# Optimization experiments

Measured on AMD Instinct MI355X. Metric: run time of the kernel, lower is better.

## Reference

```python
import jax, jax.numpy as jnp
import numpy as np

N = 8192
E = 262144
IN_DIM, HID_DIM, Z_DIM = 512, 256, 64


def setup_inputs() -> dict:
    key = jax.random.key(0)
    ks = jax.random.split(key, 8)
    x = jax.random.normal(ks[0], (N, IN_DIM), dtype=jnp.float32)
    edge_src = jax.random.randint(ks[1], (E,), 0, N, dtype=jnp.int32)
    edge_dst = jax.random.randint(ks[2], (E,), 0, N, dtype=jnp.int32)
    edge_w = jax.random.uniform(ks[3], (E,), dtype=jnp.float32)
    eps = jax.random.normal(ks[4], (N, Z_DIM), dtype=jnp.float32)
    # xavier-uniform linear weights (stored [in, out]); biases zero (as in torch init)
    def xavier(k, fan_in, fan_out):
        lim = float(np.sqrt(6.0 / (fan_in + fan_out)))
        return jax.random.uniform(k, (fan_in, fan_out), minval=-lim, maxval=lim, dtype=jnp.float32)
    W1 = xavier(ks[5], IN_DIM, HID_DIM)
    b1 = jnp.zeros((HID_DIM,), dtype=jnp.float32)
    Wmu = xavier(ks[6], HID_DIM, Z_DIM)
    bmu = jnp.zeros((Z_DIM,), dtype=jnp.float32)
    Wls = xavier(ks[7], HID_DIM, Z_DIM)
    bls = jnp.zeros((Z_DIM,), dtype=jnp.float32)
    return {"x": x, "edge_src": edge_src, "edge_dst": edge_dst, "edge_w": edge_w,
            "eps": eps, "W1": W1, "b1": b1, "Wmu": Wmu, "bmu": bmu, "Wls": Wls, "bls": bls}


def _spmm(edge_src, edge_dst, edge_w, h):
    # out[i] = sum_{(i,j) in edges} w_ij * h[j]  == torch.spmm(adj, h)
    return jax.ops.segment_sum(edge_w[:, None] * h[edge_dst], edge_src, num_segments=N)


def reference(x, edge_src, edge_dst, edge_w, eps, W1, b1, Wmu, bmu, Wls, bls):
    # GCN layer 1: linear -> spmm -> tanh
    h = jnp.tanh(_spmm(edge_src, edge_dst, edge_w, x @ W1 + b1))
    # mu / logstd heads (no activation)
    mu = _spmm(edge_src, edge_dst, edge_w, h @ Wmu + bmu)
    logstd = _spmm(edge_src, edge_dst, edge_w, h @ Wls + bls)
    # reparameterize (training mode): z = mu + eps * exp(logstd)
    z = mu + eps * jnp.exp(logstd)
    # inner-product decoder
    adj_logits = z @ z.T  # [N, N]
    return (z, adj_logits, mu, logstd)
```

## Files before the change

kernel.cpp:

```cpp
#include <hip/hip_runtime.h>
#include <math.h>

#define IN_DIM 512
#define HID    256
#define ZD     64

typedef short bf16x8 __attribute__((ext_vector_type(8)));
typedef float f32x4  __attribute__((ext_vector_type(4)));


__global__ void k_zero_int(int* p, int n) {
    int i = blockIdx.x * blockDim.x + threadIdx.x;
    if (i < n) p[i] = 0;
}

__global__ void k_count(const int* __restrict__ src, int* __restrict__ deg, int E) {
    int e = blockIdx.x * blockDim.x + threadIdx.x;
    if (e < E) atomicAdd(&deg[src[e]], 1);
}

__global__ __launch_bounds__(256) void k_scan(const int* __restrict__ deg,
                                              int* __restrict__ rp,
                                              int* __restrict__ nxt, int N) {
    __shared__ int sums[256];
    int t = threadIdx.x;
    int chunk = N / 256;
    int base = t * chunk;
    int run = 0;
    for (int i = 0; i < chunk; ++i) run += deg[base + i];
    sums[t] = run;
    __syncthreads();
    for (int off = 1; off < 256; off <<= 1) {
        int u = (t >= off) ? sums[t - off] : 0;
        __syncthreads();
        sums[t] += u;
        __syncthreads();
    }
    int excl = (t == 0) ? 0 : sums[t - 1];
    int run2 = excl;
    for (int i = 0; i < chunk; ++i) {
        rp[base + i]  = run2;
        nxt[base + i] = run2;
        run2 += deg[base + i];
    }
    if (t == 255) rp[N] = run2;
}

__global__ void k_scatter(const int* __restrict__ src, const int* __restrict__ dst,
                          const float* __restrict__ w, int* __restrict__ nxt,
                          int* __restrict__ col, float* __restrict__ wv, int E) {
    int e = blockIdx.x * blockDim.x + threadIdx.x;
    if (e < E) {
        int pos = atomicAdd(&nxt[src[e]], 1);
        col[pos] = dst[e];
        wv[pos]  = w[e];
    }
}

__global__ __launch_bounds__(256) void k_gemm1(const float* __restrict__ x,
                                               const float* __restrict__ W1,
                                               const float* __restrict__ b1,
                                               float* __restrict__ h0) {
    __shared__ float As[16][68];
    __shared__ float Bs[16][68];
    int tx = threadIdx.x, ty = threadIdx.y;
    int t = ty * 16 + tx;
    int rowBase = blockIdx.y * 64, colBase = blockIdx.x * 64;
    float acc[4][4] = {};
    int kk_l = t & 15, m0 = t >> 4;
    int c_l = t & 63, k_l = t >> 6;
    for (int k0 = 0; k0 < IN_DIM; k0 += 16) {
        #pragma unroll
        for (int p = 0; p < 4; ++p) {
            int m = m0 + p * 16;
            As[kk_l][m] = x[(size_t)(rowBase + m) * IN_DIM + k0 + kk_l];
        }
        #pragma unroll
        for (int p = 0; p < 4; ++p) {
            int kk = k_l + p * 4;
            Bs[kk][c_l] = W1[(size_t)(k0 + kk) * HID + colBase + c_l];
        }
        __syncthreads();
        #pragma unroll
        for (int kk = 0; kk < 16; ++kk) {
            float4 a4 = *(const float4*)&As[kk][ty * 4];
            float4 b4 = *(const float4*)&Bs[kk][tx * 4];
            float a[4] = {a4.x, a4.y, a4.z, a4.w};
            float b[4] = {b4.x, b4.y, b4.z, b4.w};
            #pragma unroll
            for (int r = 0; r < 4; ++r)
                #pragma unroll
                for (int c = 0; c < 4; ++c)
                    acc[r][c] += a[r] * b[c];
        }
        __syncthreads();
    }
    float4 bias = *(const float4*)&b1[colBase + tx * 4];
    float bb[4] = {bias.x, bias.y, bias.z, bias.w};
    #pragma unroll
    for (int r = 0; r < 4; ++r) {
        float4 o;
        o.x = acc[r][0] + bb[0];
        o.y = acc[r][1] + bb[1];
        o.z = acc[r][2] + bb[2];
        o.w = acc[r][3] + bb[3];
        *(float4*)&h0[(size_t)(rowBase + ty * 4 + r) * HID + colBase + tx * 4] = o;
    }
}

__global__ __launch_bounds__(256) void k_spmm_tanh(const int* __restrict__ rp,
                                                   const int* __restrict__ col,
                                                   const float* __restrict__ wv,
                                                   const float* __restrict__ h0,
                                                   float* __restrict__ h) {
    __shared__ int scol[256];
    __shared__ float sw[256];
    int i = blockIdx.x, t = threadIdx.x;
    int s = rp[i], e = rp[i + 1];
    float acc = 0.f;
    for (int cs = s; cs < e; cs += 256) {
        int n = min(256, e - cs);
        __syncthreads();
        if (t < n) { scol[t] = col[cs + t]; sw[t] = wv[cs + t]; }
        __syncthreads();
        #pragma unroll 4
        for (int p = 0; p < n; ++p)
            acc += sw[p] * h0[(size_t)scol[p] * HID + t];
    }
    h[(size_t)i * HID + t] = tanhf(acc);
}

__global__ __launch_bounds__(256) void k_heads(const float* __restrict__ h,
                                               const float* __restrict__ Wmu,
                                               const float* __restrict__ bmu,
                                               const float* __restrict__ Wls,
                                               const float* __restrict__ bls,
                                               float* __restrict__ hm,
                                               float* __restrict__ hl) {
    __shared__ float ht[16][HID + 1];
    int t = threadIdx.x;
    int rowBase = blockIdx.x * 16;
    #pragma unroll
    for (int p = 0; p < 16; ++p)
        ht[p][t] = h[(size_t)(rowBase + p) * HID + t];
    __syncthreads();
    int c = t & 63, rg = t >> 6;
    float amu[4] = {}, als[4] = {};
    #pragma unroll 4
    for (int k = 0; k < HID; ++k) {
        float wm = Wmu[k * ZD + c];
        float wl = Wls[k * ZD + c];
        #pragma unroll
        for (int r = 0; r < 4; ++r) {
            float hv = ht[rg * 4 + r][k];
            amu[r] += hv * wm;
            als[r] += hv * wl;
        }
    }
    float bm = bmu[c], bl = bls[c];
    #pragma unroll
    for (int r = 0; r < 4; ++r) {
        int row = rowBase + rg * 4 + r;
        hm[(size_t)row * ZD + c] = amu[r] + bm;
        hl[(size_t)row * ZD + c] = als[r] + bl;
    }
}

__global__ __launch_bounds__(64) void k_spmm_heads(const int* __restrict__ rp,
                                                   const int* __restrict__ col,
                                                   const float* __restrict__ wv,
                                                   const float* __restrict__ hm,
                                                   const float* __restrict__ hl,
                                                   const float* __restrict__ eps,
                                                   float* __restrict__ mu,
                                                   float* __restrict__ ls,
                                                   float* __restrict__ z) {
    __shared__ int scol[64];
    __shared__ float sw[64];
    int i = blockIdx.x, t = threadIdx.x;
    int s = rp[i], e = rp[i + 1];
    float amu = 0.f, als = 0.f;
    for (int cs = s; cs < e; cs += 64) {
        int n = min(64, e - cs);
        __syncthreads();
        if (t < n) { scol[t] = col[cs + t]; sw[t] = wv[cs + t]; }
        __syncthreads();
        #pragma unroll 4
        for (int p = 0; p < n; ++p) {
            size_t off = (size_t)scol[p] * ZD + t;
            float w = sw[p];
            amu += w * hm[off];
            als += w * hl[off];
        }
    }
    size_t o = (size_t)i * ZD + t;
    mu[o] = amu;
    ls[o] = als;
    z[o]  = amu + eps[o] * expf(als);
}

__global__ void k_cvt_bf16(const float* __restrict__ z, unsigned short* __restrict__ zb, int n4) {
    int i = blockIdx.x * blockDim.x + threadIdx.x;
    if (i < n4) {
        float4 v = *(const float4*)&z[i * 4];
        float vv[4] = {v.x, v.y, v.z, v.w};
        ushort4 o;
        unsigned short* op = (unsigned short*)&o;
        #pragma unroll
        for (int j = 0; j < 4; ++j) {
            unsigned int b = __float_as_uint(vv[j]);
            b += 0x7FFFu + ((b >> 16) & 1u);
            op[j] = (unsigned short)(b >> 16);
        }
        *(ushort4*)&zb[i * 4] = o;
    }
}

__global__ __launch_bounds__(256) void k_zzt_mfma(const unsigned short* __restrict__ zb,
                                                  float* __restrict__ out, int N) {
    int lane = threadIdx.x & 63;
    int w    = threadIdx.x >> 6;
    int waveRow = blockIdx.y * 128 + (w >> 1) * 64;
    int waveCol = blockIdx.x * 128 + (w & 1) * 64;
    int m    = lane & 15;
    int quad = lane >> 4;
    int kofs = quad * 8;

    bf16x8 a[4][2], b[4][2];
    #pragma unroll
    for (int rg = 0; rg < 4; ++rg) {
        const unsigned short* pr = zb + (size_t)(waveRow + rg * 16 + m) * ZD + kofs;
        const unsigned short* pc = zb + (size_t)(waveCol + rg * 16 + m) * ZD + kofs;
        a[rg][0] = *(const bf16x8*)pr;
        a[rg][1] = *(const bf16x8*)(pr + 32);
        b[rg][0] = *(const bf16x8*)pc;
        b[rg][1] = *(const bf16x8*)(pc + 32);
    }

    f32x4 acc[4][4] = {};
    #pragma unroll
    for (int rg = 0; rg < 4; ++rg)
        #pragma unroll
        for (int cg = 0; cg < 4; ++cg) {
            acc[rg][cg] = __builtin_amdgcn_mfma_f32_16x16x32_bf16(a[rg][0], b[cg][0], acc[rg][cg], 0, 0, 0);
            acc[rg][cg] = __builtin_amdgcn_mfma_f32_16x16x32_bf16(a[rg][1], b[cg][1], acc[rg][cg], 0, 0, 0);
        }

    #pragma unroll
    for (int rg = 0; rg < 4; ++rg) {
        int row0 = waveRow + rg * 16 + quad * 4;
        #pragma unroll
        for (int cg = 0; cg < 4; ++cg) {
            int c = waveCol + cg * 16 + m;
            #pragma unroll
            for (int r = 0; r < 4; ++r)
                out[(size_t)(row0 + r) * N + c] = acc[rg][cg][r];
        }
    }
}


extern "C" void kernel_launch(void* const* d_in, const int* in_sizes, int n_in,
                              void* d_out, int out_size, void* d_ws, size_t ws_size,
                              hipStream_t stream) {
    const float* x    = (const float*)d_in[0];
    const int*   esrc = (const int*)d_in[1];
    const int*   edst = (const int*)d_in[2];
    const float* ew   = (const float*)d_in[3];
    const float* eps  = (const float*)d_in[4];
    const float* W1   = (const float*)d_in[5];
    const float* b1   = (const float*)d_in[6];
    const float* Wmu  = (const float*)d_in[7];
    const float* bmu  = (const float*)d_in[8];
    const float* Wls  = (const float*)d_in[9];
    const float* bls  = (const float*)d_in[10];
    int N = in_sizes[0] / IN_DIM;
    int E = in_sizes[1];

    float* h0 = (float*)d_ws;
    float* h  = h0 + (size_t)N * HID;
    float* hm = h  + (size_t)N * HID;
    float* hl = hm + (size_t)N * ZD;
    int* rp   = (int*)(hl + (size_t)N * ZD);
    int* deg  = rp + (N + 1);
    int* nxt  = deg + N;
    int* col  = nxt + N;
    float* wv = (float*)(col + E);
    unsigned short* zb = (unsigned short*)(wv + E);

    float* out_z   = (float*)d_out;
    float* out_adj = out_z + (size_t)N * ZD;
    float* out_mu  = out_adj + (size_t)N * N;
    float* out_ls  = out_mu + (size_t)N * ZD;

    k_zero_int<<<(N + 255) / 256, 256, 0, stream>>>(deg, N);
    k_count<<<(E + 255) / 256, 256, 0, stream>>>(esrc, deg, E);
    k_scan<<<1, 256, 0, stream>>>(deg, rp, nxt, N);
    k_scatter<<<(E + 255) / 256, 256, 0, stream>>>(esrc, edst, ew, nxt, col, wv, E);

    dim3 b16(16, 16);
    dim3 g1(HID / 64, N / 64);
    k_gemm1<<<g1, b16, 0, stream>>>(x, W1, b1, h0);

    k_spmm_tanh<<<N, 256, 0, stream>>>(rp, col, wv, h0, h);

    k_heads<<<N / 16, 256, 0, stream>>>(h, Wmu, bmu, Wls, bls, hm, hl);

    k_spmm_heads<<<N, 64, 0, stream>>>(rp, col, wv, hm, hl, eps, out_mu, out_ls, out_z);

    k_cvt_bf16<<<(N * ZD / 4 + 255) / 256, 256, 0, stream>>>(out_z, zb, N * ZD / 4);

    dim3 g2(N / 128, N / 128);
    k_zzt_mfma<<<g2, 256, 0, stream>>>(zb, out_adj, N);
}
```

Measured before the change: 461.0 us.

## Move layer-1 GEMM to split-bf16 MFMA and fuse heads spmm with bf16 cast

Replaces the fp32 SIMT GEMM for x@W1 with a bf16x3 MFMA GEMM: x is split into hi/lo bf16 parts, W1 is transposed and split the same way, and three MFMAs per tile keep accuracy close to fp32. The mu and logstd heads are interleaved into one 128-wide buffer, so a single spmm gathers both and also writes the bf16 copy of z, which removes the separate conversion kernel. The z·zᵀ output is now written as non-temporal 16-byte vector stores using a swapped MFMA operand order. The extra split and transpose kernels add memory traffic and launch overhead in exchange.

```diff
diff --git a/kernel.cpp b/kernel.cpp
--- a/kernel.cpp
+++ b/kernel.cpp
@@ -7,6 +7,15 @@
 
 typedef short bf16x8 __attribute__((ext_vector_type(8)));
 typedef float f32x4  __attribute__((ext_vector_type(4)));
+
+__device__ inline unsigned short f2bf_rne(float f) {
+    unsigned int b = __float_as_uint(f);
+    b += 0x7FFFu + ((b >> 16) & 1u);
+    return (unsigned short)(b >> 16);
+}
+__device__ inline float bf2f(unsigned short h) {
+    return __uint_as_float(((unsigned int)h) << 16);
+}
 
 
 __global__ void k_zero_int(int* p, int n) {
@@ -57,54 +66,98 @@
     }
 }
 
-__global__ __launch_bounds__(256) void k_gemm1(const float* __restrict__ x,
-                                               const float* __restrict__ W1,
-                                               const float* __restrict__ b1,
-                                               float* __restrict__ h0) {
-    __shared__ float As[16][68];
-    __shared__ float Bs[16][68];
+__global__ void k_split_x(const float* __restrict__ x,
+                          unsigned short* __restrict__ xh,
+                          unsigned short* __restrict__ xl, int n4) {
+    int i = blockIdx.x * blockDim.x + threadIdx.x;
+    if (i < n4) {
+        float4 v = *(const float4*)&x[(size_t)i * 4];
+        float vv[4] = {v.x, v.y, v.z, v.w};
+        ushort4 ho, lo;
+        unsigned short* hp = (unsigned short*)&ho;
+        unsigned short* lp = (unsigned short*)&lo;
+        #pragma unroll
+        for (int j = 0; j < 4; ++j) {
+            unsigned short hcur = f2bf_rne(vv[j]);
+            hp[j] = hcur;
+            lp[j] = f2bf_rne(vv[j] - bf2f(hcur));
+        }
+        *(ushort4*)&xh[(size_t)i * 4] = ho;
+        *(ushort4*)&xl[(size_t)i * 4] = lo;
+    }
+}
+
+__global__ __launch_bounds__(256) void k_trans_w(const float* __restrict__ W,
+                                                 unsigned short* __restrict__ Wt_h,
+                                                 unsigned short* __restrict__ Wt_l,
+                                                 int K, int Nw) {
+    __shared__ float tile[32][33];
+    int n0 = blockIdx.x * 32, k0 = blockIdx.y * 32;
     int tx = threadIdx.x, ty = threadIdx.y;
-    int t = ty * 16 + tx;
-    int rowBase = blockIdx.y * 64, colBase = blockIdx.x * 64;
-    float acc[4][4] = {};
-    int kk_l = t & 15, m0 = t >> 4;
-    int c_l = t & 63, k_l = t >> 6;
-    for (int k0 = 0; k0 < IN_DIM; k0 += 16) {
-        #pragma unroll
-        for (int p = 0; p < 4; ++p) {
-            int m = m0 + p * 16;
-            As[kk_l][m] = x[(size_t)(rowBase + m) * IN_DIM + k0 + kk_l];
-        }
-        #pragma unroll
-        for (int p = 0; p < 4; ++p) {
-            int kk = k_l + p * 4;
-            Bs[kk][c_l] = W1[(size_t)(k0 + kk) * HID + colBase + c_l];
-        }
-        __syncthreads();
-        #pragma unroll
-        for (int kk = 0; kk < 16; ++kk) {
-            float4 a4 = *(const float4*)&As[kk][ty * 4];
-            float4 b4 = *(const float4*)&Bs[kk][tx * 4];
-            float a[4] = {a4.x, a4.y, a4.z, a4.w};
-            float b[4] = {b4.x, b4.y, b4.z, b4.w};
+    #pragma unroll
+    for (int j = 0; j < 4; ++j) {
+        int k = ty + j * 8;
+        tile[k][tx] = W[(size_t)(k0 + k) * Nw + n0 + tx];
+    }
+    __syncthreads();
+    #pragma unroll
+    for (int j = 0; j < 4; ++j) {
+        int n = ty + j * 8;
+        float v = tile[tx][n];
+        size_t o = (size_t)(n0 + n) * K + k0 + tx;
+        unsigned short hcur = f2bf_rne(v);
+        Wt_h[o] = hcur;
+        Wt_l[o] = f2bf_rne(v - bf2f(hcur));
+    }
+}
+
+__global__ __launch_bounds__(256) void k_gemm1_mfma(const unsigned short* __restrict__ xh,
+                                                    const unsigned short* __restrict__ xl,
+                                                    const unsigned short* __restrict__ wth,
+                                                    const unsigned short* __restrict__ wtl,
+                                                    const float* __restrict__ b1,
+                                                    float* __restrict__ h0) {
+    int lane = threadIdx.x & 63;
+    int w    = threadIdx.x >> 6;
+    int rowBase = blockIdx.y * 64 + (w >> 1) * 32;
+    int colBase = blockIdx.x * 64 + (w & 1) * 32;
+    int m    = lane & 15;
+    int quad = lane >> 4;
+    int kofs = quad * 8;
+
+    f32x4 acc[2][2] = {};
+    #pragma unroll 2
+    for (int k0 = 0; k0 < IN_DIM; k0 += 32) {
+        bf16x8 xhf[2], xlf[2], whf[2], wlf[2];
+        #pragma unroll
+        for (int g = 0; g < 2; ++g) {
+            size_t xoff = (size_t)(rowBase + g * 16 + m) * IN_DIM + k0 + kofs;
+            xhf[g] = *(const bf16x8*)&xh[xoff];
+            xlf[g] = *(const bf16x8*)&xl[xoff];
+            size_t woff = (size_t)(colBase + g * 16 + m) * IN_DIM + k0 + kofs;
+            whf[g] = *(const bf16x8*)&wth[woff];
+            wlf[g] = *(const bf16x8*)&wtl[woff];
+        }
+        #pragma unroll
+        for (int xg = 0; xg < 2; ++xg)
             #pragma unroll
-            for (int r = 0; r < 4; ++r)
-                #pragma unroll
-                for (int c = 0; c < 4; ++c)
-                    acc[r][c] += a[r] * b[c];
-        }
-        __syncthreads();
-    }
-    float4 bias = *(const float4*)&b1[colBase + tx * 4];
-    float bb[4] = {bias.x, bias.y, bias.z, bias.w};
-    #pragma unroll
-    for (int r = 0; r < 4; ++r) {
-        float4 o;
-        o.x = acc[r][0] + bb[0];
-        o.y = acc[r][1] + bb[1];
-        o.z = acc[r][2] + bb[2];
-        o.w = acc[r][3] + bb[3];
-        *(float4*)&h0[(size_t)(rowBase + ty * 4 + r) * HID + colBase + tx * 4] = o;
+            for (int wg = 0; wg < 2; ++wg) {
+                acc[xg][wg] = __builtin_amdgcn_mfma_f32_16x16x32_bf16(whf[wg], xhf[xg], acc[xg][wg], 0, 0, 0);
+                acc[xg][wg] = __builtin_amdgcn_mfma_f32_16x16x32_bf16(whf[wg], xlf[xg], acc[xg][wg], 0, 0, 0);
+                acc[xg][wg] = __builtin_amdgcn_mfma_f32_16x16x32_bf16(wlf[wg], xhf[xg], acc[xg][wg], 0, 0, 0);
+            }
+    }
+    #pragma unroll
+    for (int wg = 0; wg < 2; ++wg) {
+        float4 bv = *(const float4*)&b1[colBase + wg * 16 + quad * 4];
+        float bb[4] = {bv.x, bv.y, bv.z, bv.w};
+        #pragma unroll
+        for (int xg = 0; xg < 2; ++xg) {
+            f32x4 o = acc[xg][wg];
+            #pragma unroll
+            for (int r = 0; r < 4; ++r) o[r] += bb[r];
+            *(f32x4*)&h0[(size_t)(rowBase + xg * 16 + m) * HID + colBase + wg * 16 + quad * 4] = o;
+        }
     }
 }
 
@@ -135,9 +188,8 @@
                                                const float* __restrict__ bmu,
                                                const float* __restrict__ Wls,
                                                const float* __restrict__ bls,
-                                               float* __restrict__ hm,
-                                               float* __restrict__ hl) {
-    __shared__ float ht[16][HID + 1];
+                                               float* __restrict__ hh) {
+    __shared__ float ht[16][HID + 4];
     int t = threadIdx.x;
     int rowBase = blockIdx.x * 16;
     #pragma unroll
@@ -146,73 +198,65 @@
     __syncthreads();
     int c = t & 63, rg = t >> 6;
     float amu[4] = {}, als[4] = {};
-    #pragma unroll 4
-    for (int k = 0; k < HID; ++k) {
-        float wm = Wmu[k * ZD + c];
-        float wl = Wls[k * ZD + c];
+    for (int k = 0; k < HID; k += 4) {
+        float hv[4][4];
         #pragma unroll
         for (int r = 0; r < 4; ++r) {
-            float hv = ht[rg * 4 + r][k];
-            amu[r] += hv * wm;
-            als[r] += hv * wl;
+            float4 tmp = *(const float4*)&ht[rg * 4 + r][k];
+            hv[r][0] = tmp.x; hv[r][1] = tmp.y; hv[r][2] = tmp.z; hv[r][3] = tmp.w;
+        }
+        #pragma unroll
+        for (int j = 0; j < 4; ++j) {
+            float wm = Wmu[(k + j) * ZD + c];
+            float wl = Wls[(k + j) * ZD + c];
+            #pragma unroll
+            for (int r = 0; r < 4; ++r) {
+                amu[r] += hv[r][j] * wm;
+                als[r] += hv[r][j] * wl;
+            }
         }
     }
     float bm = bmu[c], bl = bls[c];
     #pragma unroll
     for (int r = 0; r < 4; ++r) {
         int row = rowBase + rg * 4 + r;
-        hm[(size_t)row * ZD + c] = amu[r] + bm;
-        hl[(size_t)row * ZD + c] = als[r] + bl;
-    }
-}
-
-__global__ __launch_bounds__(64) void k_spmm_heads(const int* __restrict__ rp,
-                                                   const int* __restrict__ col,
-                                                   const float* __restrict__ wv,
-                                                   const float* __restrict__ hm,
-                                                   const float* __restrict__ hl,
-                                                   const float* __restrict__ eps,
-                                                   float* __restrict__ mu,
-                                                   float* __restrict__ ls,
-                                                   float* __restrict__ z) {
-    __shared__ int scol[64];
-    __shared__ float sw[64];
+        hh[(size_t)row * 128 + c]      = amu[r] + bm;
+        hh[(size_t)row * 128 + 64 + c] = als[r] + bl;
+    }
+}
+
+__global__ __launch_bounds__(128) void k_spmm_heads(const int* __restrict__ rp,
+                                                    const int* __restrict__ col,
+                                                    const float* __restrict__ wv,
+                                                    const float* __restrict__ hh,
+                                                    const float* __restrict__ eps,
+                                                    float* __restrict__ mu,
+                                                    float* __restrict__ ls,
+                                                    float* __restrict__ z,
+                                                    unsigned short* __restrict__ zb) {
+    __shared__ int scol[128];
+    __shared__ float sw[128];
+    __shared__ float sls[64];
     int i = blockIdx.x, t = threadIdx.x;
     int s = rp[i], e = rp[i + 1];
-    float amu = 0.f, als = 0.f;
-    for (int cs = s; cs < e; cs += 64) {
-        int n = min(64, e - cs);
+    float acc = 0.f;
+    for (int cs = s; cs < e; cs += 128) {
+        int n = min(128, e - cs);
         __syncthreads();
         if (t < n) { scol[t] = col[cs + t]; sw[t] = wv[cs + t]; }
         __syncthreads();
         #pragma unroll 4
-        for (int p = 0; p < n; ++p) {
-            size_t off = (size_t)scol[p] * ZD + t;
-            float w = sw[p];
-            amu += w * hm[off];
-            als += w * hl[off];
-        }
-    }
-    size_t o = (size_t)i * ZD + t;
-    mu[o] = amu;
-    ls[o] = als;
-    z[o]  = amu + eps[o] * expf(als);
-}
-
-__global__ void k_cvt_bf16(const float* __restrict__ z, unsigned short* __restrict__ zb, int n4) {
-    int i = blockIdx.x * blockDim.x + threadIdx.x;
-    if (i < n4) {
-        float4 v = *(const float4*)&z[i * 4];
-        float vv[4] = {v.x, v.y, v.z, v.w};
-        ushort4 o;
-        unsigned short* op = (unsigned short*)&o;
-        #pragma unroll
-        for (int j = 0; j < 4; ++j) {
-            unsigned int b = __float_as_uint(vv[j]);
-            b += 0x7FFFu + ((b >> 16) & 1u);
-            op[j] = (unsigned short)(b >> 16);
-        }
-        *(ushort4*)&zb[i * 4] = o;
+        for (int p = 0; p < n; ++p)
+            acc += sw[p] * hh[(size_t)scol[p] * 128 + t];
+    }
+    if (t >= 64) { ls[(size_t)i * ZD + t - 64] = acc; sls[t - 64] = acc; }
+    __syncthreads();
+    if (t < 64) {
+        size_t o = (size_t)i * ZD + t;
+        mu[o] = acc;
+        float zz = acc + eps[o] * expf(sls[t]);
+        z[o] = zz;
+        zb[o] = f2bf_rne(zz);
     }
 }
 
@@ -242,19 +286,17 @@
     for (int rg = 0; rg < 4; ++rg)
         #pragma unroll
         for (int cg = 0; cg < 4; ++cg) {
-            acc[rg][cg] = __builtin_amdgcn_mfma_f32_16x16x32_bf16(a[rg][0], b[cg][0], acc[rg][cg], 0, 0, 0);
-            acc[rg][cg] = __builtin_amdgcn_mfma_f32_16x16x32_bf16(a[rg][1], b[cg][1], acc[rg][cg], 0, 0, 0);
+            acc[rg][cg] = __builtin_amdgcn_mfma_f32_16x16x32_bf16(b[cg][0], a[rg][0], acc[rg][cg], 0, 0, 0);
+            acc[rg][cg] = __builtin_amdgcn_mfma_f32_16x16x32_bf16(b[cg][1], a[rg][1], acc[rg][cg], 0, 0, 0);
         }
 
     #pragma unroll
     for (int rg = 0; rg < 4; ++rg) {
-        int row0 = waveRow + rg * 16 + quad * 4;
+        size_t rowOff = (size_t)(waveRow + rg * 16 + m) * N;
         #pragma unroll
         for (int cg = 0; cg < 4; ++cg) {
-            int c = waveCol + cg * 16 + m;
-            #pragma unroll
-            for (int r = 0; r < 4; ++r)
-                out[(size_t)(row0 + r) * N + c] = acc[rg][cg][r];
+            f32x4* po = (f32x4*)&out[rowOff + waveCol + cg * 16 + quad * 4];
+            __builtin_nontemporal_store(acc[rg][cg], po);
         }
     }
 }
@@ -277,16 +319,23 @@
     int N = in_sizes[0] / IN_DIM;
     int E = in_sizes[1];
 
-    float* h0 = (float*)d_ws;
-    float* h  = h0 + (size_t)N * HID;
-    float* hm = h  + (size_t)N * HID;
-    float* hl = hm + (size_t)N * ZD;
-    int* rp   = (int*)(hl + (size_t)N * ZD);
-    int* deg  = rp + (N + 1);
-    int* nxt  = deg + N;
-    int* col  = nxt + N;
-    float* wv = (float*)(col + E);
-    unsigned short* zb = (unsigned short*)(wv + E);
+    char* base = (char*)d_ws;
+    size_t o = 0;
+    #define ALLOC(ptr, type, count) type* ptr = (type*)(base + o); o = (o + (size_t)(count) * sizeof(type) + 63) & ~(size_t)63;
+    ALLOC(h0,  float, (size_t)N * HID)
+    ALLOC(h,   float, (size_t)N * HID)
+    ALLOC(hh,  float, (size_t)N * 128)
+    ALLOC(rp,  int,   N + 1)
+    ALLOC(deg, int,   N)
+    ALLOC(nxt, int,   N)
+    ALLOC(col, int,   E)
+    ALLOC(wv,  float, E)
+    ALLOC(zb,  unsigned short, (size_t)N * ZD)
+    ALLOC(xh,  unsigned short, (size_t)N * IN_DIM)
+    ALLOC(xl,  unsigned short, (size_t)N * IN_DIM)
+    ALLOC(wth, unsigned short, (size_t)IN_DIM * HID)
+    ALLOC(wtl, unsigned short, (size_t)IN_DIM * HID)
+    #undef ALLOC
 
     float* out_z   = (float*)d_out;
     float* out_adj = out_z + (size_t)N * ZD;
@@ -298,17 +347,17 @@
     k_scan<<<1, 256, 0, stream>>>(deg, rp, nxt, N);
     k_scatter<<<(E + 255) / 256, 256, 0, stream>>>(esrc, edst, ew, nxt, col, wv, E);
 
-    dim3 b16(16, 16);
-    dim3 g1(HID / 64, N / 64);
-    k_gemm1<<<g1, b16, 0, stream>>>(x, W1, b1, h0);
+    int n4 = N * IN_DIM / 4;
+    k_split_x<<<(n4 + 255) / 256, 256, 0, stream>>>(x, xh, xl, n4);
+    k_trans_w<<<dim3(HID / 32, IN_DIM / 32), dim3(32, 8), 0, stream>>>(W1, wth, wtl, IN_DIM, HID);
+
+    k_gemm1_mfma<<<dim3(HID / 64, N / 64), 256, 0, stream>>>(xh, xl, wth, wtl, b1, h0);
 
     k_spmm_tanh<<<N, 256, 0, stream>>>(rp, col, wv, h0, h);
 
-    k_heads<<<N / 16, 256, 0, stream>>>(h, Wmu, bmu, Wls, bls, hm, hl);
-
-    k_spmm_heads<<<N, 64, 0, stream>>>(rp, col, wv, hm, hl, eps, out_mu, out_ls, out_z);
-
-    k_cvt_bf16<<<(N * ZD / 4 + 255) / 256, 256, 0, stream>>>(out_z, zb, N * ZD / 4);
+    k_heads<<<N / 16, 256, 0, stream>>>(h, Wmu, bmu, Wls, bls, hh);
+
+    k_spmm_heads<<<N, 128, 0, stream>>>(rp, col, wv, hh, eps, out_mu, out_ls, out_z, zb);
 
     dim3 g2(N / 128, N / 128);
     k_zzt_mfma<<<g2, 256, 0, stream>>>(zb, out_adj, N);
```

Result: slower. 484.2 us (+5.0%).
